# Kernel tuning notes

Hardware: AMD Instinct MI355X
Metric: run time of the kernel (lower is better)

## Reference

```python
import math
import jax, jax.numpy as jnp
import numpy as np

B, S, D, H = 4, 2048, 1024, 16
HD = D // H  # head_dim = 64
EPS = 1e-6
LOG2_E = 1.442695041


def setup_inputs() -> dict:
    key = jax.random.key(0)
    ks = jax.random.split(key, 8)
    return {
        "inputs_q": jax.random.normal(ks[0], (B, S, D), dtype=jnp.float32),
        "Wq": jax.random.normal(ks[1], (D, D), dtype=jnp.float32) * 0.02,
        "Wk": jax.random.normal(ks[2], (D, D), dtype=jnp.float32) * 0.02,
        "Wv": jax.random.normal(ks[3], (D, D), dtype=jnp.float32) * 0.02,
        "Wo": jax.random.normal(ks[4], (D, D), dtype=jnp.float32) * 0.02,
        "q_ln_scale": jnp.ones((HD,), dtype=jnp.float32),
        "k_ln_scale": jnp.ones((HD,), dtype=jnp.float32),
        "per_dim_scale": jax.random.normal(ks[5], (HD,), dtype=jnp.float32) * 0.1,
        "patch_mask": jnp.zeros((B, S), dtype=bool),
    }


def _rope(x, position):
    # x: [B, S, H, HD], position: [B, S]
    half = HD // 2
    fraction = 2.0 * jnp.arange(half, dtype=jnp.float32) / HD
    timescale = 1.0 * (10000.0 / 1.0) ** fraction            # [half]
    sinusoid = position[:, :, None, None].astype(jnp.float32) / timescale[None, None, None, :]
    sin, cos = jnp.sin(sinusoid), jnp.cos(sinusoid)
    first, second = jnp.split(x, 2, axis=-1)
    return jnp.concatenate([first * cos - second * sin,
                            second * cos + first * sin], axis=-1)


def _rms_norm(x, scale):
    var = jnp.mean(jnp.square(x), axis=-1, keepdims=True)
    return x * jax.lax.rsqrt(var + EPS) * scale


def reference(inputs_q, Wq, Wk, Wv, Wo, q_ln_scale, k_ln_scale, per_dim_scale, patch_mask):
    b, s, d = inputs_q.shape
    # QKV projections (nn.Linear, no bias): y = x @ W.T
    q = (inputs_q @ Wq.T).reshape(b, s, H, HD)
    k = (inputs_q @ Wk.T).reshape(b, s, H, HD)
    v = (inputs_q @ Wv.T).reshape(b, s, H, HD)

    num_masked = jnp.sum(patch_mask.astype(jnp.int32), axis=-1)  # [B]
    # decode_cache=None => next_index = 0
    position = jnp.arange(s, dtype=jnp.int32)[None, :] - num_masked[:, None]  # [B, S]

    q = _rope(q, position)
    k = _rope(k, position)

    q = _rms_norm(q, q_ln_scale)
    k = _rms_norm(k, k_ln_scale)

    # per-dim scale
    q = q * (LOG2_E / math.sqrt(HD) * jax.nn.softplus(per_dim_scale))

    # causal + prefix-padding mask: [B, 1, S, S]
    q_idx = jnp.arange(s)[None, None, :, None]
    kv_idx = jnp.arange(s)[None, None, None, :]
    mask = (q_idx >= kv_idx) & (kv_idx >= num_masked[:, None, None, None])

    scores = jnp.einsum("bqhd,bkhd->bhqk", q, k)
    neg = -jnp.finfo(scores.dtype).max / 2
    scores = jnp.where(mask, scores, neg)
    attn = jax.nn.softmax(scores, axis=-1)
    x = jnp.einsum("bhqk,bkhd->bqhd", attn, v).reshape(b, s, d)
    return x @ Wo.T
```

## Files before the change

kernel.cpp:

```cpp
#include <hip/hip_runtime.h>
#include <cstdint>
#include <cstddef>

#define BB 4
#define SS 2048
#define DD 1024
#define HH 16

typedef __bf16 bf16;
typedef __bf16 bf16x8 __attribute__((ext_vector_type(8)));
typedef __bf16 bf16x4 __attribute__((ext_vector_type(4)));
typedef float f32x4 __attribute__((ext_vector_type(4)));
typedef unsigned int u32;

typedef __attribute__((address_space(1))) const void* as1_cvoid;
typedef __attribute__((address_space(3))) void* as3_void;

__device__ __forceinline__ void gload_lds16(const void* g, void* l) {
  __builtin_amdgcn_global_load_lds((as1_cvoid)g, (as3_void)l, 16, 0, 0);
}

__global__ void mask_count_kernel(const unsigned char* __restrict__ mask, int* __restrict__ nm) {
  int wid = threadIdx.x >> 6, lane = threadIdx.x & 63;
  if (wid >= BB) return;
  int s = 0;
  for (int i = lane; i < SS; i += 64) s += (mask[wid * SS + i] != 0) ? 1 : 0;
#pragma unroll
  for (int m = 1; m < 64; m <<= 1) s += __shfl_xor(s, m);
  if (lane == 0) nm[wid] = s;
}

__global__ void cvt_kernel(const float* __restrict__ src, bf16* __restrict__ dst, int n4) {
  int stride = gridDim.x * blockDim.x;
  for (int i = blockIdx.x * blockDim.x + threadIdx.x; i < n4; i += stride) {
    float4 v = ((const float4*)src)[i];
    bf16x4 o;
    o[0] = (bf16)v.x; o[1] = (bf16)v.y; o[2] = (bf16)v.z; o[3] = (bf16)v.w;
    ((bf16x4*)dst)[i] = o;
  }
}

__global__ void sincos_table_kernel(const int* __restrict__ nm, float2* __restrict__ tbl) {
  int g = blockIdx.x * 256 + threadIdx.x;
  int j = g & 31;
  int idx = g >> 5;
  int b = idx >> 11, s = idx & 2047;
  int pos = s - nm[b];
  float inv_ts = __expf((float)j * (-9.210340371976184f / 32.0f));
  float sn, cs;
  sincosf((float)pos * inv_ts, &sn, &cs);
  tbl[g] = make_float2(cs, sn);
}

__global__ void __launch_bounds__(256) gemm_qkv_kernel(
    const bf16* __restrict__ A, const bf16* __restrict__ Wq, const bf16* __restrict__ Wk,
    const bf16* __restrict__ Wv, const float* __restrict__ qls, const float* __restrict__ kls,
    const float* __restrict__ pds, const float2* __restrict__ tbl,
    bf16* __restrict__ Qp, bf16* __restrict__ Kp, bf16* __restrict__ Vt) {
  __shared__ __align__(16) char smem[4 * 64 * 72 * 2];
  bf16* Ab = (bf16*)smem;
  bf16* Bb = (bf16*)(smem + 8192);
  const int tid = threadIdx.x;
  const int wid = tid >> 6, lane = tid & 63;
  const int lr = lane & 15, lg = lane >> 4;
  const int K = DD;
  const int nx = 24;
  const int cpx = gridDim.x >> 3;
  const int lid = (blockIdx.x & 7) * cpx + (blockIdx.x >> 3);
  const int m0 = (lid / nx) * 128;
  const int ntile = lid % nx;
  const int which = ntile >> 3;
  const int n0 = (ntile & 7) * 128;
  const bf16* Bm = which == 0 ? Wq : (which == 1 ? Wk : Wv);
  const int wm = (wid >> 1) * 64, wn = (wid & 1) * 64;
  f32x4 acc[4][4] = {};
  for (int k0 = 0; k0 < K; k0 += 32) {
    __syncthreads();
#pragma unroll
    for (int i = 0; i < 2; ++i) {
      int o = (wid * 2 + i) * 1024 + lane * 16;
      int row = o >> 6;
      int ke = (o & 63) >> 1;
      gload_lds16(A + (size_t)(m0 + row) * K + k0 + ke, (char*)Ab + o);
      gload_lds16(Bm + (size_t)(n0 + row) * K + k0 + ke, (char*)Bb + o);
    }
    __syncthreads();
    bf16x8 af[4], bf_[4];
#pragma unroll
    for (int i = 0; i < 4; ++i) af[i] = *(const bf16x8*)&Ab[(wm + i * 16 + lr) * 32 + lg * 8];
#pragma unroll
    for (int j = 0; j < 4; ++j) bf_[j] = *(const bf16x8*)&Bb[(wn + j * 16 + lr) * 32 + lg * 8];
#pragma unroll
    for (int i = 0; i < 4; ++i)
#pragma unroll
      for (int j = 0; j < 4; ++j)
        acc[i][j] = __builtin_amdgcn_mfma_f32_16x16x32_bf16(af[i], bf_[j], acc[i][j], 0, 0, 0);
  }
  const int b = m0 >> 11;
  const int s0g = m0 & 2047;
  const int hq = n0 >> 6;
  if (which < 2) {
    float scj[4];
#pragma unroll
    for (int j = 0; j < 4; ++j) {
      int d = j * 16 + lr;
      scj[j] = (which == 0) ? qls[d] * 0.26017112262570096f * log1pf(__expf(pds[d]))
                            : kls[d];
    }
    bf16* Out = which == 0 ? Qp : Kp;
    const int h = hq + (wn >> 6);
    const size_t base = (size_t)(b * 16 + h) * SS;
#pragma unroll
    for (int i = 0; i < 4; ++i)
#pragma unroll
      for (int r = 0; r < 4; ++r) {
        int srow = s0g + wm + i * 16 + lg * 4 + r;
        const float2* trow = tbl + ((size_t)(b * SS + srow) << 5);
        float2 t0 = trow[lr], t1 = trow[16 + lr];
        float a0 = acc[i][0][r], a1 = acc[i][1][r], a2 = acc[i][2][r], a3 = acc[i][3][r];
        float n0_ = a0 * t0.x - a2 * t0.y;
        float n2_ = a2 * t0.x + a0 * t0.y;
        float n1_ = a1 * t1.x - a3 * t1.y;
        float n3_ = a3 * t1.x + a1 * t1.y;
        float ssum = n0_ * n0_ + n1_ * n1_ + n2_ * n2_ + n3_ * n3_;
        ssum += __shfl_xor(ssum, 1);
        ssum += __shfl_xor(ssum, 2);
        ssum += __shfl_xor(ssum, 4);
        ssum += __shfl_xor(ssum, 8);
        float rinv = rsqrtf(ssum * (1.0f / 64.0f) + 1e-6f);
        bf16* orow = Out + (base + srow) * 64;
        orow[lr]      = (bf16)(n0_ * rinv * scj[0]);
        orow[16 + lr] = (bf16)(n1_ * rinv * scj[1]);
        orow[32 + lr] = (bf16)(n2_ * rinv * scj[2]);
        orow[48 + lr] = (bf16)(n3_ * rinv * scj[3]);
      }
  } else {
    __syncthreads();
    bf16* tw = (bf16*)smem + wid * 64 * 72;
#pragma unroll
    for (int i = 0; i < 4; ++i)
#pragma unroll
      for (int j = 0; j < 4; ++j)
#pragma unroll
        for (int r = 0; r < 4; ++r)
          tw[(j * 16 + lr) * 72 + i * 16 + lg * 4 + r] = (bf16)acc[i][j][r];
    __syncthreads();
    int d = tid >> 2, sc = (tid & 3) * 16;
#pragma unroll
    for (int w = 0; w < 4; ++w) {
      int rh = w >> 1, hh = w & 1;
      const bf16* ts = (const bf16*)smem + w * 64 * 72 + d * 72 + sc;
      bf16x8 v0 = *(const bf16x8*)ts;
      bf16x8 v1 = *(const bf16x8*)(ts + 8);
      size_t vo = ((size_t)((b * 16 + hq + hh) * 64 + d)) * SS + s0g + rh * 64 + sc;
      *(bf16x8*)(Vt + vo) = v0;
      *(bf16x8*)(Vt + vo + 8) = v1;
    }
  }
}

__global__ void __launch_bounds__(256) gemm_bt_kernel(const bf16* __restrict__ A,
                                                      const bf16* __restrict__ Bm,
                                                      float* __restrict__ Cout,
                                                      int M, int N, int K) {
  __shared__ bf16 Ab[128 * 32];
  __shared__ bf16 Bb[128 * 32];
  const int tid = threadIdx.x;
  const int wid = tid >> 6, lane = tid & 63;
  const int lr = lane & 15, lg = lane >> 4;
  const int nx = N >> 7;
  const int cpx = gridDim.x >> 3;
  const int lid = (blockIdx.x & 7) * cpx + (blockIdx.x >> 3);
  const int m0 = (lid / nx) * 128, n0 = (lid % nx) * 128;
  const int wm = (wid >> 1) * 64, wn = (wid & 1) * 64;
  f32x4 acc[4][4] = {};
  for (int k0 = 0; k0 < K; k0 += 32) {
    __syncthreads();
#pragma unroll
    for (int i = 0; i < 2; ++i) {
      int o = (wid * 2 + i) * 1024 + lane * 16;
      int row = o >> 6;
      int ke = (o & 63) >> 1;
      gload_lds16(A + (size_t)(m0 + row) * K + k0 + ke, (char*)Ab + o);
      gload_lds16(Bm + (size_t)(n0 + row) * K + k0 + ke, (char*)Bb + o);
    }
    __syncthreads();
    bf16x8 af[4], bf_[4];
#pragma unroll
    for (int i = 0; i < 4; ++i) af[i] = *(const bf16x8*)&Ab[(wm + i * 16 + lr) * 32 + lg * 8];
#pragma unroll
    for (int j = 0; j < 4; ++j) bf_[j] = *(const bf16x8*)&Bb[(wn + j * 16 + lr) * 32 + lg * 8];
#pragma unroll
    for (int i = 0; i < 4; ++i)
#pragma unroll
      for (int j = 0; j < 4; ++j)
        acc[i][j] = __builtin_amdgcn_mfma_f32_16x16x32_bf16(af[i], bf_[j], acc[i][j], 0, 0, 0);
  }
#pragma unroll
  for (int i = 0; i < 4; ++i)
#pragma unroll
    for (int j = 0; j < 4; ++j)
#pragma unroll
      for (int r = 0; r < 4; ++r) {
        int row = m0 + wm + i * 16 + lg * 4 + r;
        int col = n0 + wn + j * 16 + lr;
        Cout[(size_t)row * N + col] = acc[i][j][r];
      }
}

__global__ void __launch_bounds__(256, 2) flash_kernel(
    const bf16* __restrict__ Qp, const bf16* __restrict__ Kp, const bf16* __restrict__ Vt,
    bf16* __restrict__ O, const int* __restrict__ nm) {
  __shared__ bf16 Kb[2][64 * 64];
  __shared__ bf16 Vb[64 * 64];
  __shared__ u32 Pl[4][16][36];
  const int bh = blockIdx.x & 63;
  const int px = blockIdx.x >> 6;
  const int xA = 31 - px, xB = px;
  const int b = bh >> 4, h = bh & 15;
  const int tid = threadIdx.x;
  const int wid = tid >> 6, lane = tid & 63;
  const int lr = lane & 15, lg = lane >> 4;
  const int nmb = nm[b];
  const int wqA = xA * 64 + wid * 16;
  const int wqB = xB * 64 + wid * 16;
  const int nt = xA + 1;

  bf16x8 qfA[2], qfB[2];
#pragma unroll
  for (int kh = 0; kh < 2; ++kh) {
    qfA[kh] = *(const bf16x8*)(Qp + ((size_t)bh * SS + wqA + lr) * 64 + kh * 32 + lg * 8);
    qfB[kh] = *(const bf16x8*)(Qp + ((size_t)bh * SS + wqB + lr) * 64 + kh * 32 + lg * 8);
  }

  float mA = -1e30f, lA = 0.f, mB = -1e30f, lB = 0.f;
  f32x4 oA[4] = {}, oB[4] = {};

  auto STAGE_K = [&](int bi, int t) {
    const int kv0 = t * 64;
#pragma unroll
    for (int i = 0; i < 2; ++i) {
      int o = i * 4096 + tid * 16;
      int row = o >> 7;
      int c16 = ((o >> 4) & 7) ^ (row & 7);
      gload_lds16(Kp + ((size_t)bh * SS + kv0 + row) * 64 + c16 * 8, (char*)Kb[bi] + o);
    }
  };
  auto STAGE_V = [&](int t) {
    const int kv0 = t * 64;
#pragma unroll
    for (int i = 0; i < 2; ++i) {
      int o = i * 4096 + tid * 16;
      int row = o >> 7;
      int c16 = ((o >> 4) & 7) ^ (row & 7);
      gload_lds16(Vt + ((size_t)bh * 64 + row) * SS + kv0 + c16 * 8, (char*)Vb + o);
    }
  };

  STAGE_K(0, 0);
  STAGE_V(0);
  __syncthreads();
  int buf = 0;
  for (int t = 0; t < nt; ++t) {
    const int kv0 = t * 64;
    if (t + 1 < nt) STAGE_K(buf ^ 1, t + 1);
    const bool actB = (t <= xB);
    bf16x8 pbA[2], pbB[2];
    f32x4 sA[4], sB[4];

    __builtin_amdgcn_s_setprio(1);
#pragma unroll
    for (int j = 0; j < 4; ++j) {
      int row = j * 16 + lr;
      const char* kbase = (const char*)Kb[buf] + row * 128;
      bf16x8 kf0 = *(const bf16x8*)(kbase + ((lg ^ (row & 7)) << 4));
      bf16x8 kf1 = *(const bf16x8*)(kbase + (((4 + lg) ^ (row & 7)) << 4));
      f32x4 z = {};
      z = __builtin_amdgcn_mfma_f32_16x16x32_bf16(kf0, qfA[0], z, 0, 0, 0);
      z = __builtin_amdgcn_mfma_f32_16x16x32_bf16(kf1, qfA[1], z, 0, 0, 0);
      sA[j] = z;
      if (actB) {
        f32x4 z2 = {};
        z2 = __builtin_amdgcn_mfma_f32_16x16x32_bf16(kf0, qfB[0], z2, 0, 0, 0);
        z2 = __builtin_amdgcn_mfma_f32_16x16x32_bf16(kf1, qfB[1], z2, 0, 0, 0);
        sB[j] = z2;
      }
    }
    __builtin_amdgcn_s_setprio(0);

    auto SOFTMAX = [&](f32x4* s, float& m_r, float& l_pp, f32x4* oacc, bf16x8* pb,
                       int xS, int wqS) {
      if (t == xS) {
        int qr = wqS + lr;
#pragma unroll
        for (int j = 0; j < 4; ++j) {
          int kvb = kv0 + j * 16 + lg * 4;
#pragma unroll
          for (int r = 0; r < 4; ++r)
            if (kvb + r > qr) s[j][r] = -1e30f;
        }
      }
      if (kv0 < nmb) {
#pragma unroll
        for (int j = 0; j < 4; ++j) {
          int kvb = kv0 + j * 16 + lg * 4;
#pragma unroll
          for (int r = 0; r < 4; ++r)
            if (kvb + r < nmb) s[j][r] = -1e30f;
        }
      }
      float t0 = fmaxf(fmaxf(s[0][0], s[0][1]), s[0][2]);
      float t1 = fmaxf(fmaxf(s[0][3], s[1][0]), s[1][1]);
      float t2 = fmaxf(fmaxf(s[1][2], s[1][3]), s[2][0]);
      float t3 = fmaxf(fmaxf(s[2][1], s[2][2]), s[2][3]);
      float t4 = fmaxf(fmaxf(s[3][0], s[3][1]), s[3][2]);
      float t5 = fmaxf(fmaxf(t0, t1), s[3][3]);
      float pm = fmaxf(fmaxf(t2, t3), fmaxf(t4, t5));
      if (!__all(pm - m_r <= 8.f)) {
        pm = fmaxf(pm, __shfl_xor(pm, 16));
        pm = fmaxf(pm, __shfl_xor(pm, 32));
        float mn = fmaxf(m_r, pm);
        float scl = exp2f(m_r - mn);
        m_r = mn;
        l_pp *= scl;
        f32x4 sv = {scl, scl, scl, scl};
#pragma unroll
        for (int jd = 0; jd < 4; ++jd) oacc[jd] *= sv;
      }
      const float mloc = m_r;
      float lp = l_pp;
#pragma unroll
      for (int j = 0; j < 4; ++j) {
        float p0 = exp2f(s[j][0] - mloc), p1 = exp2f(s[j][1] - mloc);
        float p2 = exp2f(s[j][2] - mloc), p3 = exp2f(s[j][3] - mloc);
        lp += (p0 + p1) + (p2 + p3);
        union { bf16 hx[4]; uint2 u2; } pk;
        pk.hx[0] = (bf16)p0; pk.hx[1] = (bf16)p1;
        pk.hx[2] = (bf16)p2; pk.hx[3] = (bf16)p3;
        *(uint2*)&Pl[wid][lr][j * 8 + lg * 2] = pk.u2;
      }
      l_pp = lp;
#pragma unroll
      for (int kh = 0; kh < 2; ++kh) pb[kh] = *(const bf16x8*)&Pl[wid][lr][kh * 16 + lg * 4];
    };

    SOFTMAX(sA, mA, lA, oA, pbA, xA, wqA);
    if (actB) SOFTMAX(sB, mB, lB, oB, pbB, xB, wqB);

    if (t > 0) {
      if (t + 1 < nt)
        asm volatile("s_waitcnt vmcnt(2)" ::: "memory");
      else
        asm volatile("s_waitcnt vmcnt(0)" ::: "memory");
      __builtin_amdgcn_s_barrier();
      __builtin_amdgcn_sched_barrier(0);
    }
    __builtin_amdgcn_s_setprio(1);
#pragma unroll
    for (int jd = 0; jd < 4; ++jd) {
      int row = jd * 16 + lr;
      const char* vbase = (const char*)Vb + row * 128;
      bf16x8 va0 = *(const bf16x8*)(vbase + ((lg ^ (row & 7)) << 4));
      bf16x8 va1 = *(const bf16x8*)(vbase + (((4 + lg) ^ (row & 7)) << 4));
      oA[jd] = __builtin_amdgcn_mfma_f32_16x16x32_bf16(va0, pbA[0], oA[jd], 0, 0, 0);
      oA[jd] = __builtin_amdgcn_mfma_f32_16x16x32_bf16(va1, pbA[1], oA[jd], 0, 0, 0);
      if (actB) {
        oB[jd] = __builtin_amdgcn_mfma_f32_16x16x32_bf16(va0, pbB[0], oB[jd], 0, 0, 0);
        oB[jd] = __builtin_amdgcn_mfma_f32_16x16x32_bf16(va1, pbB[1], oB[jd], 0, 0, 0);
      }
    }
    __builtin_amdgcn_s_setprio(0);
    __syncthreads();
    if (t + 1 < nt) STAGE_V(t + 1);
    buf ^= 1;
  }
#pragma unroll
  for (int st = 0; st < 2; ++st) {
    float l = st == 0 ? lA : lB;
    const f32x4* oacc = st == 0 ? oA : oB;
    int wq = st == 0 ? wqA : wqB;
    l += __shfl_xor(l, 16);
    l += __shfl_xor(l, 32);
    float invl = 1.0f / l;
    size_t rowoff = ((size_t)b * SS + wq + lr) * DD + h * 64;
#pragma unroll
    for (int jd = 0; jd < 4; ++jd) {
      f32x4 ov = oacc[jd] * invl;
      bf16x4 hv;
      hv[0] = (bf16)ov[0]; hv[1] = (bf16)ov[1]; hv[2] = (bf16)ov[2]; hv[3] = (bf16)ov[3];
      *(bf16x4*)(O + rowoff + jd * 16 + lg * 4) = hv;
    }
  }
}

extern "C" void kernel_launch(void* const* d_in, const int* in_sizes, int n_in,
                              void* d_out, int out_size, void* d_ws, size_t ws_size,
                              hipStream_t stream) {
  const float* X = (const float*)d_in[0];
  const float* Wq = (const float*)d_in[1];
  const float* Wk = (const float*)d_in[2];
  const float* Wv = (const float*)d_in[3];
  const float* Wo = (const float*)d_in[4];
  const float* qls = (const float*)d_in[5];
  const float* kls = (const float*)d_in[6];
  const float* pds = (const float*)d_in[7];
  const unsigned char* mask = (const unsigned char*)d_in[8];

  char* ws = (char*)d_ws;
  size_t off = 0;
  auto alloc = [&](size_t bytes) {
    char* p = ws + off;
    off += (bytes + 255) & ~(size_t)255;
    return p;
  };
  const size_t NTOK = (size_t)BB * SS;
  int* nm = (int*)alloc(16);
  bf16* Xb = (bf16*)alloc(NTOK * DD * 2);
  bf16* Wqb = (bf16*)alloc((size_t)DD * DD * 2);
  bf16* Wkb = (bf16*)alloc((size_t)DD * DD * 2);
  bf16* Wvb = (bf16*)alloc((size_t)DD * DD * 2);
  bf16* Wob = (bf16*)alloc((size_t)DD * DD * 2);
  bf16* Qp = (bf16*)alloc(NTOK * DD * 2);
  bf16* Kp = (bf16*)alloc(NTOK * DD * 2);
  bf16* Vt = (bf16*)alloc(NTOK * DD * 2);
  float2* tbl = (float2*)alloc(NTOK * 32 * sizeof(float2));
  bf16* Oat = Xb;

  mask_count_kernel<<<1, 256, 0, stream>>>(mask, nm);
  cvt_kernel<<<1024, 256, 0, stream>>>(X, Xb, (int)(NTOK * DD / 4));
  cvt_kernel<<<256, 256, 0, stream>>>(Wq, Wqb, DD * DD / 4);
  cvt_kernel<<<256, 256, 0, stream>>>(Wk, Wkb, DD * DD / 4);
  cvt_kernel<<<256, 256, 0, stream>>>(Wv, Wvb, DD * DD / 4);
  cvt_kernel<<<256, 256, 0, stream>>>(Wo, Wob, DD * DD / 4);
  sincos_table_kernel<<<1024, 256, 0, stream>>>(nm, tbl);

  gemm_qkv_kernel<<<(int)(NTOK / 128) * 24, 256, 0, stream>>>(Xb, Wqb, Wkb, Wvb, qls, kls, pds,
                                                              tbl, Qp, Kp, Vt);
  flash_kernel<<<1024, 256, 0, stream>>>(Qp, Kp, Vt, Oat, nm);
  gemm_bt_kernel<<<(int)(NTOK / 128) * (DD / 128), 256, 0, stream>>>(Oat, Wob, (float*)d_out,
                                                                     (int)NTOK, DD, DD);
}
```

Measured before the change: 199.8 us.

## Double-buffer V tiles in flash attention and merge weight conversions

The flash attention kernel now double-buffers V alongside K, prefetching both for the next tile at the start of each iteration. This removes the mid-iteration wait and barrier before PV, leaving one wait-and-barrier at the end. PV for query block A is interleaved right after its softmax, before block B's softmax. The four weight conversion launches are merged into one kernel; in exchange, LDS use grows by 8 KB per block, which may lower occupancy.

```diff
diff --git a/kernel.cpp b/kernel.cpp
--- a/kernel.cpp
+++ b/kernel.cpp
@@ -33,6 +33,22 @@
 __global__ void cvt_kernel(const float* __restrict__ src, bf16* __restrict__ dst, int n4) {
   int stride = gridDim.x * blockDim.x;
   for (int i = blockIdx.x * blockDim.x + threadIdx.x; i < n4; i += stride) {
+    float4 v = ((const float4*)src)[i];
+    bf16x4 o;
+    o[0] = (bf16)v.x; o[1] = (bf16)v.y; o[2] = (bf16)v.z; o[3] = (bf16)v.w;
+    ((bf16x4*)dst)[i] = o;
+  }
+}
+
+__global__ void cvt4_kernel(const float* __restrict__ W0, const float* __restrict__ W1,
+                            const float* __restrict__ W2, const float* __restrict__ W3,
+                            bf16* __restrict__ D0, bf16* __restrict__ D1,
+                            bf16* __restrict__ D2, bf16* __restrict__ D3) {
+  int which = blockIdx.x >> 8;
+  const float* src = which == 0 ? W0 : which == 1 ? W1 : which == 2 ? W2 : W3;
+  bf16* dst = which == 0 ? D0 : which == 1 ? D1 : which == 2 ? D2 : D3;
+  const int n4 = DD * DD / 4;
+  for (int i = (blockIdx.x & 255) * 256 + threadIdx.x; i < n4; i += 65536) {
     float4 v = ((const float4*)src)[i];
     bf16x4 o;
     o[0] = (bf16)v.x; o[1] = (bf16)v.y; o[2] = (bf16)v.z; o[3] = (bf16)v.w;
@@ -212,7 +228,7 @@
     const bf16* __restrict__ Qp, const bf16* __restrict__ Kp, const bf16* __restrict__ Vt,
     bf16* __restrict__ O, const int* __restrict__ nm) {
   __shared__ bf16 Kb[2][64 * 64];
-  __shared__ bf16 Vb[64 * 64];
+  __shared__ bf16 Vb[2][64 * 64];
   __shared__ u32 Pl[4][16][36];
   const int bh = blockIdx.x & 63;
   const int px = blockIdx.x >> 6;
@@ -236,7 +252,7 @@
   float mA = -1e30f, lA = 0.f, mB = -1e30f, lB = 0.f;
   f32x4 oA[4] = {}, oB[4] = {};
 
-  auto STAGE_K = [&](int bi, int t) {
+  auto STAGE = [&](int bi, int t) {
     const int kv0 = t * 64;
 #pragma unroll
     for (int i = 0; i < 2; ++i) {
@@ -244,28 +260,19 @@
       int row = o >> 7;
       int c16 = ((o >> 4) & 7) ^ (row & 7);
       gload_lds16(Kp + ((size_t)bh * SS + kv0 + row) * 64 + c16 * 8, (char*)Kb[bi] + o);
+      gload_lds16(Vt + ((size_t)bh * 64 + row) * SS + kv0 + c16 * 8, (char*)Vb[bi] + o);
     }
   };
-  auto STAGE_V = [&](int t) {
-    const int kv0 = t * 64;
-#pragma unroll
-    for (int i = 0; i < 2; ++i) {
-      int o = i * 4096 + tid * 16;
-      int row = o >> 7;
-      int c16 = ((o >> 4) & 7) ^ (row & 7);
-      gload_lds16(Vt + ((size_t)bh * 64 + row) * SS + kv0 + c16 * 8, (char*)Vb + o);
-    }
-  };
-
-  STAGE_K(0, 0);
-  STAGE_V(0);
-  __syncthreads();
+
+  STAGE(0, 0);
+  asm volatile("s_waitcnt vmcnt(0)" ::: "memory");
+  __builtin_amdgcn_s_barrier();
+  __builtin_amdgcn_sched_barrier(0);
   int buf = 0;
   for (int t = 0; t < nt; ++t) {
     const int kv0 = t * 64;
-    if (t + 1 < nt) STAGE_K(buf ^ 1, t + 1);
+    if (t + 1 < nt) STAGE(buf ^ 1, t + 1);
     const bool actB = (t <= xB);
-    bf16x8 pbA[2], pbB[2];
     f32x4 sA[4], sB[4];
 
     __builtin_amdgcn_s_setprio(1);
@@ -344,34 +351,30 @@
       for (int kh = 0; kh < 2; ++kh) pb[kh] = *(const bf16x8*)&Pl[wid][lr][kh * 16 + lg * 4];
     };
 
+    auto PV = [&](f32x4* oacc, bf16x8* pb) {
+      __builtin_amdgcn_s_setprio(1);
+#pragma unroll
+      for (int jd = 0; jd < 4; ++jd) {
+        int row = jd * 16 + lr;
+        const char* vbase = (const char*)Vb[buf] + row * 128;
+        bf16x8 va0 = *(const bf16x8*)(vbase + ((lg ^ (row & 7)) << 4));
+        bf16x8 va1 = *(const bf16x8*)(vbase + (((4 + lg) ^ (row & 7)) << 4));
+        oacc[jd] = __builtin_amdgcn_mfma_f32_16x16x32_bf16(va0, pb[0], oacc[jd], 0, 0, 0);
+        oacc[jd] = __builtin_amdgcn_mfma_f32_16x16x32_bf16(va1, pb[1], oacc[jd], 0, 0, 0);
+      }
+      __builtin_amdgcn_s_setprio(0);
+    };
+
+    bf16x8 pbA[2], pbB[2];
     SOFTMAX(sA, mA, lA, oA, pbA, xA, wqA);
-    if (actB) SOFTMAX(sB, mB, lB, oB, pbB, xB, wqB);
-
-    if (t > 0) {
-      if (t + 1 < nt)
-        asm volatile("s_waitcnt vmcnt(2)" ::: "memory");
-      else
-        asm volatile("s_waitcnt vmcnt(0)" ::: "memory");
-      __builtin_amdgcn_s_barrier();
-      __builtin_amdgcn_sched_barrier(0);
-    }
-    __builtin_amdgcn_s_setprio(1);
-#pragma unroll
-    for (int jd = 0; jd < 4; ++jd) {
-      int row = jd * 16 + lr;
-      const char* vbase = (const char*)Vb + row * 128;
-      bf16x8 va0 = *(const bf16x8*)(vbase + ((lg ^ (row & 7)) << 4));
-      bf16x8 va1 = *(const bf16x8*)(vbase + (((4 + lg) ^ (row & 7)) << 4));
-      oA[jd] = __builtin_amdgcn_mfma_f32_16x16x32_bf16(va0, pbA[0], oA[jd], 0, 0, 0);
-      oA[jd] = __builtin_amdgcn_mfma_f32_16x16x32_bf16(va1, pbA[1], oA[jd], 0, 0, 0);
-      if (actB) {
-        oB[jd] = __builtin_amdgcn_mfma_f32_16x16x32_bf16(va0, pbB[0], oB[jd], 0, 0, 0);
-        oB[jd] = __builtin_amdgcn_mfma_f32_16x16x32_bf16(va1, pbB[1], oB[jd], 0, 0, 0);
-      }
-    }
-    __builtin_amdgcn_s_setprio(0);
-    __syncthreads();
-    if (t + 1 < nt) STAGE_V(t + 1);
+    PV(oA, pbA);
+    if (actB) {
+      SOFTMAX(sB, mB, lB, oB, pbB, xB, wqB);
+      PV(oB, pbB);
+    }
+    asm volatile("s_waitcnt vmcnt(0)" ::: "memory");
+    __builtin_amdgcn_s_barrier();
+    __builtin_amdgcn_sched_barrier(0);
     buf ^= 1;
   }
 #pragma unroll
@@ -428,10 +431,7 @@
 
   mask_count_kernel<<<1, 256, 0, stream>>>(mask, nm);
   cvt_kernel<<<1024, 256, 0, stream>>>(X, Xb, (int)(NTOK * DD / 4));
-  cvt_kernel<<<256, 256, 0, stream>>>(Wq, Wqb, DD * DD / 4);
-  cvt_kernel<<<256, 256, 0, stream>>>(Wk, Wkb, DD * DD / 4);
-  cvt_kernel<<<256, 256, 0, stream>>>(Wv, Wvb, DD * DD / 4);
-  cvt_kernel<<<256, 256, 0, stream>>>(Wo, Wob, DD * DD / 4);
+  cvt4_kernel<<<1024, 256, 0, stream>>>(Wq, Wk, Wv, Wo, Wqb, Wkb, Wvb, Wob);
   sincos_table_kernel<<<1024, 256, 0, stream>>>(nm, tbl);
 
   gemm_qkv_kernel<<<(int)(NTOK / 128) * 24, 256, 0, stream>>>(Xb, Wqb, Wkb, Wvb, qls, kls, pds,
```

Measured after the change: 204.7 us. 2.5% more time.
